# Performance work log

Measured on AMD Instinct MI355X. Metric: run time of the kernel, lower is better.

Reference implementation:

```python
import jax, jax.numpy as jnp
import numpy as np
import math

N = 9                 # board side (9x9 Go board)
C = N * N             # number of board coords == number of stone slots
STONE_VALUE = 1.0     # init kwarg: predicted stone colour
DIST_LT_W, DIST_LIN_W = 0.5, 0.5
ANGLE_LT_W, ANGLE_LIN_W = 45.0, 0.5


def setup_inputs() -> dict:
    key = jax.random.key(0)
    # board values in {-1, 0, +1}
    board = (jax.random.randint(key, (N, N), 0, 3) - 1).astype(jnp.float32)
    ys, xs = jnp.meshgrid(jnp.arange(N, dtype=jnp.int32), jnp.arange(N, dtype=jnp.int32), indexing='ij')
    all_coords = jnp.stack([board.reshape(-1).astype(jnp.int32), ys.reshape(-1), xs.reshape(-1)], axis=1)  # [C,3] rows [value,y,x]
    return {"all_coords": all_coords, "board": board}


def _influence_totals(all_coords, board):
    # ---- candidate-independent geometry (GetStoneDistAngle3d) ----
    yx = all_coords[:, 1:].astype(jnp.float32)                # [C,2]
    d = yx[None, :, :] - yx[:, None, :]                       # stone - coord, [C,S,2]
    dist = jnp.sqrt(d[..., 0] ** 2 + d[..., 1] ** 2)          # [C,S]
    raw = jnp.arctan2(-d[..., 0], d[..., 1]) * (180.0 / math.pi)
    angle = jnp.where(raw > 0, raw, raw + 360.0)              # 360-degree angles, (0 -> 360)
    order = jnp.argsort(dist, axis=1)                         # sort stones by dist per coord (sort2dByCol)
    dist_s = jnp.take_along_axis(dist, order, axis=1)         # [C,S]
    angle_s = jnp.take_along_axis(angle, order, axis=1)       # [C,S]

    # ---- base influence: max_dist - dist, normalize to [0,1], dist bias ----
    max_dist = jnp.float32(math.sqrt(2.0) * N)                # ||[N,N]||
    base = (max_dist - dist_s) / max_dist
    base = jnp.where(base < DIST_LT_W, base * DIST_LIN_W, base)  # ApplyLtLinWeight1d

    # ---- angle-bias pair mask (candidate-independent part) ----
    ad = jnp.abs(angle_s[:, :, None] - angle_s[:, None, :])   # [C,S,S]
    ad = jnp.where(ad > 180.0, 360.0 - ad, ad)
    tri = jnp.arange(C)[:, None] < jnp.arange(C)[None, :]      # i < j (outer def i, inner agr j)
    A = ((ad < ANGLE_LT_W) & tri[None, :, :]).astype(jnp.float32)  # [C,S,S]

    # ---- per-candidate stone placement (GetInflPredictions3d.predInfl) ----
    bf = board.reshape(-1)                                    # [S]
    empty = bf == 0
    boardp = bf[None, :] + jnp.eye(C, dtype=bf.dtype) * STONE_VALUE  # [B,S], B == C candidates
    s = boardp[:, order]                                      # [B,C,S] dist-sorted stone values

    # opposing-stone pair indicator: 1 iff s_i * s_j == -1 (both stones present, different colour)
    M = jax.nn.relu(-(s[:, :, :, None] * s[:, :, None, :]))   # [B,C,S,S]
    # number of earlier (closer) opposing stones within 45 deg -> each halves the influence
    k = jnp.einsum('cij,bcij->bcj', A, M)                     # [B,C,S]
    infl = base[None] * jnp.exp(k * jnp.log(jnp.float32(ANGLE_LIN_W))) * s
    coord_infl = infl.sum(-1)                                 # [B,C] per-coord influence
    coord_infl = jnp.where(boardp == 0, coord_infl, 0.0)      # only empty coords have influence
    total = coord_infl.sum(-1)                                # [B] net board influence per candidate
    return jnp.where(empty, total, 0.0)                       # non-empty candidates -> 0


def reference(all_coords, board):
    return _influence_totals(all_coords, board)
```

## Files before the change

kernel.cpp:

```cpp
#include <hip/hip_runtime.h>
#include <math.h>


#define C 81
#define NB 9

__global__ __launch_bounds__(128) void infl_kernel(const float* __restrict__ board,
                                                   float* __restrict__ out) {
    const int c = blockIdx.x;
    const int t = threadIdx.x;
    const int wave = t >> 6;

    __shared__ float s_bf[C];
    __shared__ int   s_key[C];
    __shared__ float s_ang[C];
    __shared__ float s_base[C];
    __shared__ unsigned long long s_maskLo[C], s_maskHi[C];
    __shared__ unsigned long long s_pos[2], s_neg[2];

    const int yc = c / NB, xc = c % NB;

    float bv = 0.0f;
    if (t < C) {
        bv = board[t];
        s_bf[t] = bv;
        const int dy = t / NB - yc, dx = t % NB - xc;
        s_key[t] = (dy * dy + dx * dx) * 128 + t;

        const float d0 = (float)dy, d1 = (float)dx;
        const float dist = sqrtf(d0 * d0 + d1 * d1);
        const float MAXD = 12.727922061357855f;
        float base = (MAXD - dist) / MAXD;
        if (base < 0.5f) base *= 0.5f;
        s_base[t] = base;

        const float nd0 = -d0;
        const float a32 = (float)atan2((double)nd0, (double)d1);
        const float raw = a32 * 57.29577951308232f;
        s_ang[t] = (raw > 0.0f) ? raw : (raw + 360.0f);
    }
    const unsigned long long bp = __ballot(bv > 0.0f);
    const unsigned long long bn = __ballot(bv < 0.0f);
    if ((t & 63) == 0) { s_pos[wave] = bp; s_neg[wave] = bn; }
    __syncthreads();

    if (s_bf[c] != 0.0f) return;

    if (t < C) {
        const int v = t;
        const float av = s_ang[v];
        const int   kv = s_key[v];
        unsigned long long lo = 0ull, hi = 0ull;
        for (int u = 0; u < C; ++u) {
            float ad = fabsf(s_ang[u] - av);
            if (ad > 180.0f) ad = 360.0f - ad;
            if ((ad < 45.0f) & (s_key[u] < kv)) {
                if (u < 64) lo |= 1ull << u; else hi |= 1ull << (u - 64);
            }
        }
        s_maskLo[v] = lo;
        s_maskHi[v] = hi;
    }
    __syncthreads();

    if (t < C) {
        const int b = t;
        if (b != c && s_bf[b] == 0.0f) {
            const unsigned long long pLo = s_pos[0] | ((b < 64) ? (1ull << b) : 0ull);
            const unsigned long long pHi = s_pos[1] | ((b >= 64) ? (1ull << (b - 64)) : 0ull);
            const unsigned long long nLo = s_neg[0];
            const unsigned long long nHi = s_neg[1];
            float sum = 0.0f;
            for (unsigned long long m = pLo | nLo; m; m &= m - 1) {
                const int j = __builtin_ctzll(m);
                const bool isneg = (nLo >> j) & 1ull;
                const unsigned long long oLo = isneg ? pLo : nLo;
                const unsigned long long oHi = isneg ? pHi : nHi;
                const int cnt = __popcll(s_maskLo[j] & oLo) + __popcll(s_maskHi[j] & oHi);
                const float term = ldexpf(s_base[j], -cnt);
                sum += isneg ? -term : term;
            }
            for (unsigned long long m = pHi | nHi; m; m &= m - 1) {
                const int jb = __builtin_ctzll(m);
                const int j = jb + 64;
                const bool isneg = (nHi >> jb) & 1ull;
                const unsigned long long oLo = isneg ? pLo : nLo;
                const unsigned long long oHi = isneg ? pHi : nHi;
                const int cnt = __popcll(s_maskLo[j] & oLo) + __popcll(s_maskHi[j] & oHi);
                const float term = ldexpf(s_base[j], -cnt);
                sum += isneg ? -term : term;
            }
            atomicAdd(&out[b], sum);
        }
    }
}

extern "C" void kernel_launch(void* const* d_in, const int* in_sizes, int n_in,
                              void* d_out, int out_size, void* d_ws, size_t ws_size,
                              hipStream_t stream) {
    const float* board = (const float*)d_in[1];
    float* out = (float*)d_out;

    infl_kernel<<<C, 128, 0, stream>>>(board, out);
}
```

Baseline: 72.55 us.

## Decompose per-candidate influence into board-constant sum plus local correction

Replaces the per-pair bitmask construction and per-candidate full recount with an algebraic decomposition. Each existing stone's influence without a candidate is computed once per coordinate and reduced across the block into a constant. Each candidate then only adds its own stone term and halves the terms of negative stones it shadows, which are found by scanning only the negative stones. This cuts the O(C^2) mask build and popcount loops, at the cost of a wave-shuffle reduction and correctness that depends on STONE_VALUE being +1.

```diff
diff --git a/kernel.cpp b/kernel.cpp
--- a/kernel.cpp
+++ b/kernel.cpp
@@ -15,8 +15,9 @@
     __shared__ int   s_key[C];
     __shared__ float s_ang[C];
     __shared__ float s_base[C];
-    __shared__ unsigned long long s_maskLo[C], s_maskHi[C];
+    __shared__ float s_t0[C];
     __shared__ unsigned long long s_pos[2], s_neg[2];
+    __shared__ float s_red[2][2];
 
     const int yc = c / NB, xc = c % NB;
 
@@ -46,50 +47,71 @@
 
     if (s_bf[c] != 0.0f) return;
 
-    if (t < C) {
-        const int v = t;
-        const float av = s_ang[v];
-        const int   kv = s_key[v];
-        unsigned long long lo = 0ull, hi = 0ull;
-        for (int u = 0; u < C; ++u) {
-            float ad = fabsf(s_ang[u] - av);
+    const unsigned long long pLo = s_pos[0], pHi = s_pos[1];
+    const unsigned long long nLo = s_neg[0], nHi = s_neg[1];
+
+    float sp = 0.0f, sn = 0.0f;
+    if (t < C && bv != 0.0f) {
+        const float av = s_ang[t];
+        const int   kv = s_key[t];
+        const bool vneg = bv < 0.0f;
+        int cnt = 0;
+        for (unsigned long long m = pLo | nLo; m; m &= m - 1) {
+            const int j = __builtin_ctzll(m);
+            const bool jneg = (nLo >> j) & 1ull;
+            float ad = fabsf(s_ang[j] - av);
             if (ad > 180.0f) ad = 360.0f - ad;
-            if ((ad < 45.0f) & (s_key[u] < kv)) {
-                if (u < 64) lo |= 1ull << u; else hi |= 1ull << (u - 64);
-            }
+            cnt += ((jneg != vneg) & (ad < 45.0f) & (s_key[j] < kv)) ? 1 : 0;
         }
-        s_maskLo[v] = lo;
-        s_maskHi[v] = hi;
+        for (unsigned long long m = pHi | nHi; m; m &= m - 1) {
+            const int jb = __builtin_ctzll(m);
+            const int j = jb + 64;
+            const bool jneg = (nHi >> jb) & 1ull;
+            float ad = fabsf(s_ang[j] - av);
+            if (ad > 180.0f) ad = 360.0f - ad;
+            cnt += ((jneg != vneg) & (ad < 45.0f) & (s_key[j] < kv)) ? 1 : 0;
+        }
+        const float t0 = ldexpf(s_base[t], -cnt);
+        s_t0[t] = t0;
+        if (vneg) sn = t0; else sp = t0;
     }
+    for (int off = 32; off; off >>= 1) {
+        sp += __shfl_xor(sp, off);
+        sn += __shfl_xor(sn, off);
+    }
+    if ((t & 63) == 0) { s_red[wave][0] = sp; s_red[wave][1] = sn; }
     __syncthreads();
+
+    const float Sconst = (s_red[0][0] + s_red[1][0]) - (s_red[0][1] + s_red[1][1]);
 
     if (t < C) {
         const int b = t;
-        if (b != c && s_bf[b] == 0.0f) {
-            const unsigned long long pLo = s_pos[0] | ((b < 64) ? (1ull << b) : 0ull);
-            const unsigned long long pHi = s_pos[1] | ((b >= 64) ? (1ull << (b - 64)) : 0ull);
-            const unsigned long long nLo = s_neg[0];
-            const unsigned long long nHi = s_neg[1];
-            float sum = 0.0f;
-            for (unsigned long long m = pLo | nLo; m; m &= m - 1) {
+        if (b != c && bv == 0.0f) {
+            const float ab = s_ang[b];
+            const int   kb = s_key[b];
+            float W = 0.0f;
+            int cntb = 0;
+            for (unsigned long long m = nLo; m; m &= m - 1) {
                 const int j = __builtin_ctzll(m);
-                const bool isneg = (nLo >> j) & 1ull;
-                const unsigned long long oLo = isneg ? pLo : nLo;
-                const unsigned long long oHi = isneg ? pHi : nHi;
-                const int cnt = __popcll(s_maskLo[j] & oLo) + __popcll(s_maskHi[j] & oHi);
-                const float term = ldexpf(s_base[j], -cnt);
-                sum += isneg ? -term : term;
+                float ad = fabsf(s_ang[j] - ab);
+                if (ad > 180.0f) ad = 360.0f - ad;
+                if (ad < 45.0f) {
+                    if (s_key[j] < kb) cntb++;
+                    else               W += s_t0[j];
+                }
             }
-            for (unsigned long long m = pHi | nHi; m; m &= m - 1) {
-                const int jb = __builtin_ctzll(m);
-                const int j = jb + 64;
-                const bool isneg = (nHi >> jb) & 1ull;
-                const unsigned long long oLo = isneg ? pLo : nLo;
-                const unsigned long long oHi = isneg ? pHi : nHi;
-                const int cnt = __popcll(s_maskLo[j] & oLo) + __popcll(s_maskHi[j] & oHi);
-                const float term = ldexpf(s_base[j], -cnt);
-                sum += isneg ? -term : term;
+            for (unsigned long long m = nHi; m; m &= m - 1) {
+                const int jb2 = __builtin_ctzll(m);
+                const int j = jb2 + 64;
+                float ad = fabsf(s_ang[j] - ab);
+                if (ad > 180.0f) ad = 360.0f - ad;
+                if (ad < 45.0f) {
+                    if (s_key[j] < kb) cntb++;
+                    else               W += s_t0[j];
+                }
             }
+            const float own = ldexpf(s_base[b], -cntb);
+            const float sum = Sconst + 0.5f * W + own;
             atomicAdd(&out[b], sum);
         }
     }
```

Measured after the change: 66.99 us. 7.7% less time.

## Restructure influence sum by decomposing candidate effect into constant plus per-stone corrections

Applied to the files above, without the earlier changes.

The per-coord pairwise angle masks over all 81 slots are no longer built. Each thread now scans only the occupied stones: for existing stones it counts nearer opposing stones in the cone, and for empty slots it records which negative stones it would shadow. A block reduction produces the candidate-independent stone sum, and each candidate adds halved corrections plus its own term. The early exit moves before shared setup, which removes a quadratic loop and a second mask pass but relies on a subtle algebraic decomposition that assumes the placed stone value is positive.

```diff
diff --git a/kernel.cpp b/kernel.cpp
--- a/kernel.cpp
+++ b/kernel.cpp
@@ -11,21 +11,23 @@
     const int t = threadIdx.x;
     const int wave = t >> 6;
 
-    __shared__ float s_bf[C];
-    __shared__ int   s_key[C];
-    __shared__ float s_ang[C];
+    if (board[c] != 0.0f) return;
+
+    __shared__ float s_ak[2 * C];
     __shared__ float s_base[C];
-    __shared__ unsigned long long s_maskLo[C], s_maskHi[C];
+    __shared__ float s_t0[C];
     __shared__ unsigned long long s_pos[2], s_neg[2];
+    __shared__ float s_red[2];
 
     const int yc = c / NB, xc = c % NB;
 
     float bv = 0.0f;
+    float av = 0.0f;
+    int   kv = 0;
     if (t < C) {
         bv = board[t];
-        s_bf[t] = bv;
         const int dy = t / NB - yc, dx = t % NB - xc;
-        s_key[t] = (dy * dy + dx * dx) * 128 + t;
+        kv = (dy * dy + dx * dx) * 128 + t;
 
         const float d0 = (float)dy, d1 = (float)dx;
         const float dist = sqrtf(d0 * d0 + d1 * d1);
@@ -37,61 +39,76 @@
         const float nd0 = -d0;
         const float a32 = (float)atan2((double)nd0, (double)d1);
         const float raw = a32 * 57.29577951308232f;
-        s_ang[t] = (raw > 0.0f) ? raw : (raw + 360.0f);
+        av = (raw > 0.0f) ? raw : (raw + 360.0f);
+        s_ak[2 * t]     = av;
+        s_ak[2 * t + 1] = __int_as_float(kv);
     }
     const unsigned long long bp = __ballot(bv > 0.0f);
     const unsigned long long bn = __ballot(bv < 0.0f);
     if ((t & 63) == 0) { s_pos[wave] = bp; s_neg[wave] = bn; }
     __syncthreads();
 
-    if (s_bf[c] != 0.0f) return;
+    const unsigned long long pLo = s_pos[0], pHi = s_pos[1];
+    const unsigned long long nLo = s_neg[0], nHi = s_neg[1];
 
-    if (t < C) {
-        const int v = t;
-        const float av = s_ang[v];
-        const int   kv = s_key[v];
-        unsigned long long lo = 0ull, hi = 0ull;
-        for (int u = 0; u < C; ++u) {
-            float ad = fabsf(s_ang[u] - av);
-            if (ad > 180.0f) ad = 360.0f - ad;
-            if ((ad < 45.0f) & (s_key[u] < kv)) {
-                if (u < 64) lo |= 1ull << u; else hi |= 1ull << (u - 64);
-            }
+    const bool isStone = (bv != 0.0f);
+    const bool vneg    = (bv < 0.0f);
+
+    int cnt = 0, cntb = 0;
+    unsigned long long wmLo = 0ull, wmHi = 0ull;
+    for (unsigned long long m = pLo | nLo; m; m &= m - 1) {
+        const int j = __builtin_ctzll(m);
+        const bool jneg = (nLo >> j) & 1ull;
+        const float aj = s_ak[2 * j];
+        const int   kj = __float_as_int(s_ak[2 * j + 1]);
+        float ad = fabsf(aj - av);
+        if (ad > 180.0f) ad = 360.0f - ad;
+        const bool cone   = ad < 45.0f;
+        const bool nearer = kj < kv;
+        if (isStone) {
+            cnt += (cone & nearer & (jneg != vneg)) ? 1 : 0;
+        } else if (jneg) {
+            if (cone & nearer) cntb++;
+            if (cone & !nearer) wmLo |= 1ull << j;
         }
-        s_maskLo[v] = lo;
-        s_maskHi[v] = hi;
     }
+    for (unsigned long long m = pHi | nHi; m; m &= m - 1) {
+        const int jb = __builtin_ctzll(m);
+        const int j  = jb + 64;
+        const bool jneg = (nHi >> jb) & 1ull;
+        const float aj = s_ak[2 * j];
+        const int   kj = __float_as_int(s_ak[2 * j + 1]);
+        float ad = fabsf(aj - av);
+        if (ad > 180.0f) ad = 360.0f - ad;
+        const bool cone   = ad < 45.0f;
+        const bool nearer = kj < kv;
+        if (isStone) {
+            cnt += (cone & nearer & (jneg != vneg)) ? 1 : 0;
+        } else if (jneg) {
+            if (cone & nearer) cntb++;
+            if (cone & !nearer) wmHi |= 1ull << jb;
+        }
+    }
+
+    float t0s = 0.0f;
+    if (isStone) {
+        const float t0 = ldexpf(s_base[t], -cnt);
+        s_t0[t] = t0;
+        t0s = vneg ? -t0 : t0;
+    }
+    for (int off = 32; off; off >>= 1) t0s += __shfl_xor(t0s, off);
+    if ((t & 63) == 0) s_red[wave] = t0s;
     __syncthreads();
 
-    if (t < C) {
-        const int b = t;
-        if (b != c && s_bf[b] == 0.0f) {
-            const unsigned long long pLo = s_pos[0] | ((b < 64) ? (1ull << b) : 0ull);
-            const unsigned long long pHi = s_pos[1] | ((b >= 64) ? (1ull << (b - 64)) : 0ull);
-            const unsigned long long nLo = s_neg[0];
-            const unsigned long long nHi = s_neg[1];
-            float sum = 0.0f;
-            for (unsigned long long m = pLo | nLo; m; m &= m - 1) {
-                const int j = __builtin_ctzll(m);
-                const bool isneg = (nLo >> j) & 1ull;
-                const unsigned long long oLo = isneg ? pLo : nLo;
-                const unsigned long long oHi = isneg ? pHi : nHi;
-                const int cnt = __popcll(s_maskLo[j] & oLo) + __popcll(s_maskHi[j] & oHi);
-                const float term = ldexpf(s_base[j], -cnt);
-                sum += isneg ? -term : term;
-            }
-            for (unsigned long long m = pHi | nHi; m; m &= m - 1) {
-                const int jb = __builtin_ctzll(m);
-                const int j = jb + 64;
-                const bool isneg = (nHi >> jb) & 1ull;
-                const unsigned long long oLo = isneg ? pLo : nLo;
-                const unsigned long long oHi = isneg ? pHi : nHi;
-                const int cnt = __popcll(s_maskLo[j] & oLo) + __popcll(s_maskHi[j] & oHi);
-                const float term = ldexpf(s_base[j], -cnt);
-                sum += isneg ? -term : term;
-            }
-            atomicAdd(&out[b], sum);
-        }
+    if (t < C && t != c && !isStone) {
+        const float Sconst = s_red[0] + s_red[1];
+        float W = 0.0f;
+        for (unsigned long long m = wmLo; m; m &= m - 1)
+            W += s_t0[__builtin_ctzll(m)];
+        for (unsigned long long m = wmHi; m; m &= m - 1)
+            W += s_t0[64 + __builtin_ctzll(m)];
+        const float own = ldexpf(s_base[t], -cntb);
+        atomicAdd(&out[t], Sconst + 0.5f * W + own);
     }
 }
 
```

Result: faster. 64.99 us (-10.4%).
